# Kernel tuning notes

Hardware: AMD Instinct MI355X
Metric: run time of the kernel (lower is better)

## Reference

```python
import jax, jax.numpy as jnp
import numpy as np

B, M, H, D, C = 512, 40, 128, 64, 128


def setup_inputs() -> dict:
    key = jax.random.key(0)
    k1, k2, k3, k4 = jax.random.split(key, 4)
    x0 = jax.random.normal(k1, (B, M, D), dtype=jnp.float32)
    xk = jax.random.normal(k2, (B, H, D), dtype=jnp.float32)
    # Conv1d(kernel_size=1) weight [C, H*M, 1] squeezed to [C, H*M]; bias [C]
    W = jax.random.normal(k3, (C, H * M), dtype=jnp.float32) * 0.02
    b = jax.random.normal(k4, (C,), dtype=jnp.float32) * 0.02
    return {"x0": x0, "xk": xk, "W": W, "b": b}


def reference(x0, xk, W, b):
    # torch: outer[b, h*M+m, d] = xk[b,h,d] * x0[b,m,d]; out = conv1d(outer)
    # conv1d with kernel_size=1 is a channel contraction:
    #   out[b,c,d] = sum_{h,m} W[c, h*M+m] * xk[b,h,d] * x0[b,m,d] + b[c]
    Bsz, Hh, Dd = xk.shape
    Mm = x0.shape[1]
    Cc = W.shape[0]
    Wr = W.reshape(Cc, Hh, Mm)  # channel index is h*M + m -> [C, H, M]
    out = jnp.einsum('bhd,bmd,chm->bcd', xk, x0, Wr) + b[None, :, None]
    return out  # [B, C, D]
```

## Files before the change

### kernel.cpp

```cpp
#include <hip/hip_runtime.h>
#include <hip/hip_bf16.h>

typedef __attribute__((ext_vector_type(8))) short short8;
typedef __attribute__((ext_vector_type(4))) float f32x4;
typedef unsigned short u16;
typedef unsigned int u32;

#define NB 512
#define NM 40
#define NH 128
#define ND 64
#define NC 128
#define KTOT 5120
#define XKP 136
#define X0P 72

__device__ __forceinline__ u16 f2bf_rne(float f) {
    u32 u = __float_as_uint(f);
    u32 r = u + 0x7FFFu + ((u >> 16) & 1u);
    return (u16)(r >> 16);
}
__device__ __forceinline__ float bf2f(short s) {
    return __uint_as_float(((u32)(u16)s) << 16);
}

__device__ __forceinline__ short8 bmul(float s, short8 xv) {
    union { short8 s8; u32 u4[4]; } r;
#pragma unroll
    for (int j = 0; j < 4; ++j) {
        float f0 = s * bf2f(xv[2 * j]);
        float f1 = s * bf2f(xv[2 * j + 1]);
        r.u4[j] = __builtin_amdgcn_perm(__float_as_uint(f1), __float_as_uint(f0),
                                        0x07060302u);
    }
    return r.s8;
}

__global__ void w3_kernel(const float* __restrict__ W, u16* __restrict__ W3) {
    __shared__ u16 kbuf[KTOT];
    const int c = blockIdx.x;
    const float* src = W + (size_t)c * KTOT;
    for (int k = threadIdx.x; k < KTOT; k += 256)
        kbuf[k] = f2bf_rne(src[k]);
    __syncthreads();
    for (int n8 = threadIdx.x; n8 < 640; n8 += 256) {
        int m = n8 % 40, hh = n8 / 40;
        union { short8 s8; u16 e[8]; } v;
#pragma unroll
        for (int j = 0; j < 8; ++j)
            v.e[j] = kbuf[hh * 320 + j * 40 + m];
        int t = n8 >> 2, q = n8 & 3;
        *(short8*)(W3 + (size_t)t * 4096 + q * 1024 + c * 8) = v.s8;
    }
}

__global__ void __launch_bounds__(256) cin_main(
    const float* __restrict__ x0g, const float* __restrict__ xkg,
    const float* __restrict__ biasg, const u16* __restrict__ W3,
    float* __restrict__ out)
{
    __shared__ __align__(16) char smem[62208];
    short* A2     = (short*)smem;
    short* xkT    = (short*)(smem + 32768);
    float* x0s    = (float*)(smem + 50176);
    float* bias_s = (float*)(smem + 61696);
    float* red    = (float*)smem;

    const int tid = threadIdx.x;
    const int b = blockIdx.x;
    const int w = tid >> 6, L = tid & 63;
    const int q = L >> 4, l16 = L & 15;
    const int kh = w >> 1;
    const int rh = w & 1;

    {
        const float* xp = xkg + (size_t)b * (NH * ND);
        for (int i = tid; i < 2048; i += 256) {
            int h = i >> 4, d4 = (i & 15) << 2;
            float4 v = *(const float4*)(xp + h * ND + d4);
            xkT[(d4 + 0) * XKP + h] = f2bf_rne(v.x);
            xkT[(d4 + 1) * XKP + h] = f2bf_rne(v.y);
            xkT[(d4 + 2) * XKP + h] = f2bf_rne(v.z);
            xkT[(d4 + 3) * XKP + h] = f2bf_rne(v.w);
        }
        const float* x0p = x0g + (size_t)b * (NM * ND);
        for (int i = tid; i < 640; i += 256) {
            int m = i >> 4, d4 = (i & 15) << 2;
            *(f32x4*)(x0s + m * X0P + d4) = *(const f32x4*)(x0p + m * ND + d4);
        }
        if (tid < NC) bias_s[tid] = biasg[tid];
    }

    auto stage = [&](int tt1, int bufb) {
        const int tglob = kh * 80 + tt1;
#pragma unroll
        for (int r = 0; r < 4; ++r) {
            const int n = rh * 4 + r;
            const u16* g = W3 + (size_t)tglob * 4096 + n * 512 + L * 8;
            short* dst = A2 + bufb * 8192 + kh * 4096 + n * 512;
            __builtin_amdgcn_global_load_lds(
                (const __attribute__((address_space(1))) void*)g,
                (__attribute__((address_space(3))) void*)dst, 16, 0, 0);
        }
    };

    stage(0, 0);

    f32x4 acc[4][4] = {};
    short8 xv[4];

    for (int tp = 0; tp < 8; ++tp) {
        const int hh = kh * 8 + tp;
#pragma unroll
        for (int n = 0; n < 4; ++n)
            xv[n] = *(const short8*)&xkT[(n * 16 + l16) * XKP + hh * 8];
#pragma unroll 2
        for (int ti = 0; ti < 10; ++ti) {
            const int tt = tp * 10 + ti;
            __syncthreads();
            if (tt + 1 < 80) stage(tt + 1, (tt + 1) & 1);
            const short* Ab = A2 + (tt & 1) * 8192 + kh * 4096 +
                              q * 1024 + (rh * 64 + l16) * 8;
            const float* px0 = x0s + (4 * ti + q) * X0P + l16;
            short8 a0 = *(const short8*)(Ab);
            short8 a1 = *(const short8*)(Ab + 128);
            short8 a2 = *(const short8*)(Ab + 256);
            short8 a3 = *(const short8*)(Ab + 384);
#pragma unroll
            for (int n = 0; n < 4; ++n) {
                short8 bf = bmul(px0[n * 16], xv[n]);
                acc[0][n] = __builtin_amdgcn_mfma_f32_16x16x32_bf16(a0, bf, acc[0][n], 0, 0, 0);
                acc[1][n] = __builtin_amdgcn_mfma_f32_16x16x32_bf16(a1, bf, acc[1][n], 0, 0, 0);
                acc[2][n] = __builtin_amdgcn_mfma_f32_16x16x32_bf16(a2, bf, acc[2][n], 0, 0, 0);
                acc[3][n] = __builtin_amdgcn_mfma_f32_16x16x32_bf16(a3, bf, acc[3][n], 0, 0, 0);
            }
        }
    }

    __syncthreads();
    float* r0 = red + rh * 4352;
    if (kh == 1) {
#pragma unroll
        for (int mt = 0; mt < 4; ++mt)
#pragma unroll
            for (int rr = 0; rr < 4; ++rr) {
                int row = mt * 16 + q * 4 + rr;
                float* p = r0 + row * 68 + l16;
                p[0]  = acc[mt][0][rr];
                p[16] = acc[mt][1][rr];
                p[32] = acc[mt][2][rr];
                p[48] = acc[mt][3][rr];
            }
    }
    __syncthreads();
    if (kh == 0) {
        float* op = out + (size_t)b * (NC * ND);
#pragma unroll
        for (int mt = 0; mt < 4; ++mt)
#pragma unroll
            for (int rr = 0; rr < 4; ++rr) {
                int row = mt * 16 + q * 4 + rr;
                int c = rh * 64 + row;
                const float* p = r0 + row * 68 + l16;
                float bv = bias_s[c];
                op[c * ND + 0  + l16] = acc[mt][0][rr] + p[0]  + bv;
                op[c * ND + 16 + l16] = acc[mt][1][rr] + p[16] + bv;
                op[c * ND + 32 + l16] = acc[mt][2][rr] + p[32] + bv;
                op[c * ND + 48 + l16] = acc[mt][3][rr] + p[48] + bv;
            }
    }
}

extern "C" void kernel_launch(void* const* d_in, const int* in_sizes, int n_in,
                              void* d_out, int out_size, void* d_ws, size_t ws_size,
                              hipStream_t stream) {
    const float* x0 = (const float*)d_in[0];
    const float* xk = (const float*)d_in[1];
    const float* W  = (const float*)d_in[2];
    const float* bi = (const float*)d_in[3];
    float* out = (float*)d_out;

    u16* W3 = (u16*)d_ws;

    w3_kernel<<<NC, 256, 0, stream>>>(W, W3);
    cin_main<<<NB, 256, 0, stream>>>(x0, xk, bi, W3, out);
}
```

Baseline: 125.1 us.

## Load W fragments directly into registers with prefetch, drop LDS staging

Replaces the double-buffered global-to-LDS staging of the bf16 weight tiles with direct per-lane global loads into registers, prefetching the next tile while the current one feeds the MFMAs. This removes the per-iteration __syncthreads and the LDS round trip. It also shrinks shared memory and adds a launch-bounds occupancy hint of 2 blocks per CU. The cost is redundant global/L2 traffic, since each wave now fetches its own fragments, and higher register pressure from the prefetch buffers.

```diff
diff --git a/kernel.cpp b/kernel.cpp
--- a/kernel.cpp
+++ b/kernel.cpp
@@ -54,16 +54,15 @@
     }
 }
 
-__global__ void __launch_bounds__(256) cin_main(
+__global__ void __launch_bounds__(256, 2) cin_main(
     const float* __restrict__ x0g, const float* __restrict__ xkg,
     const float* __restrict__ biasg, const u16* __restrict__ W3,
     float* __restrict__ out)
 {
-    __shared__ __align__(16) char smem[62208];
-    short* A2     = (short*)smem;
-    short* xkT    = (short*)(smem + 32768);
-    float* x0s    = (float*)(smem + 50176);
-    float* bias_s = (float*)(smem + 61696);
+    __shared__ __align__(16) char smem[35328];
+    short* xkT    = (short*)smem;
+    float* x0s    = (float*)(smem + 17408);
+    float* bias_s = (float*)(smem + 34816);
     float* red    = (float*)smem;
 
     const int tid = threadIdx.x;
@@ -72,6 +71,16 @@
     const int q = L >> 4, l16 = L & 15;
     const int kh = w >> 1;
     const int rh = w & 1;
+
+    const u16* Ap = W3 + q * 1024 + (size_t)(rh * 64 + l16) * 8;
+    auto loadA = [&](int t, short8* a) {
+#pragma unroll
+        for (int mt = 0; mt < 4; ++mt)
+            a[mt] = *(const short8*)(Ap + (size_t)t * 4096 + mt * 128);
+    };
+
+    short8 aC[4], aN[4];
+    loadA(kh * 80, aC);
 
     {
         const float* xp = xkg + (size_t)b * (NH * ND);
@@ -90,21 +99,7 @@
         }
         if (tid < NC) bias_s[tid] = biasg[tid];
     }
-
-    auto stage = [&](int tt1, int bufb) {
-        const int tglob = kh * 80 + tt1;
-#pragma unroll
-        for (int r = 0; r < 4; ++r) {
-            const int n = rh * 4 + r;
-            const u16* g = W3 + (size_t)tglob * 4096 + n * 512 + L * 8;
-            short* dst = A2 + bufb * 8192 + kh * 4096 + n * 512;
-            __builtin_amdgcn_global_load_lds(
-                (const __attribute__((address_space(1))) void*)g,
-                (__attribute__((address_space(3))) void*)dst, 16, 0, 0);
-        }
-    };
-
-    stage(0, 0);
+    __syncthreads();
 
     f32x4 acc[4][4] = {};
     short8 xv[4];
@@ -117,23 +112,19 @@
 #pragma unroll 2
         for (int ti = 0; ti < 10; ++ti) {
             const int tt = tp * 10 + ti;
-            __syncthreads();
-            if (tt + 1 < 80) stage(tt + 1, (tt + 1) & 1);
-            const short* Ab = A2 + (tt & 1) * 8192 + kh * 4096 +
-                              q * 1024 + (rh * 64 + l16) * 8;
+            const int tn = (tt + 1 < 80) ? (kh * 80 + tt + 1) : kh * 80;
+            loadA(tn, aN);
             const float* px0 = x0s + (4 * ti + q) * X0P + l16;
-            short8 a0 = *(const short8*)(Ab);
-            short8 a1 = *(const short8*)(Ab + 128);
-            short8 a2 = *(const short8*)(Ab + 256);
-            short8 a3 = *(const short8*)(Ab + 384);
 #pragma unroll
             for (int n = 0; n < 4; ++n) {
                 short8 bf = bmul(px0[n * 16], xv[n]);
-                acc[0][n] = __builtin_amdgcn_mfma_f32_16x16x32_bf16(a0, bf, acc[0][n], 0, 0, 0);
-                acc[1][n] = __builtin_amdgcn_mfma_f32_16x16x32_bf16(a1, bf, acc[1][n], 0, 0, 0);
-                acc[2][n] = __builtin_amdgcn_mfma_f32_16x16x32_bf16(a2, bf, acc[2][n], 0, 0, 0);
-                acc[3][n] = __builtin_amdgcn_mfma_f32_16x16x32_bf16(a3, bf, acc[3][n], 0, 0, 0);
+                acc[0][n] = __builtin_amdgcn_mfma_f32_16x16x32_bf16(aC[0], bf, acc[0][n], 0, 0, 0);
+                acc[1][n] = __builtin_amdgcn_mfma_f32_16x16x32_bf16(aC[1], bf, acc[1][n], 0, 0, 0);
+                acc[2][n] = __builtin_amdgcn_mfma_f32_16x16x32_bf16(aC[2], bf, acc[2][n], 0, 0, 0);
+                acc[3][n] = __builtin_amdgcn_mfma_f32_16x16x32_bf16(aC[3], bf, acc[3][n], 0, 0, 0);
             }
+#pragma unroll
+            for (int mt = 0; mt < 4; ++mt) aC[mt] = aN[mt];
         }
     }
 
```

New measurement: 120.3 us. 1.04x faster.
